# Performance work log

Hardware: AMD Instinct MI355X
Metric: run time of the kernel (lower is better)

Reference implementation:

```python
import jax, jax.numpy as jnp
import numpy as np
from jax import lax

OUT_SCALE = 0.001


def setup_inputs() -> dict:
    key = jax.random.key(0)
    kz, kx = jax.random.split(key)
    z = jax.random.normal(kz, (64, 256, 7, 7), dtype=jnp.float32)
    x = jax.random.normal(kx, (64, 256, 31, 31), dtype=jnp.float32)
    return {"z": z, "x": x}


def reference(z, x):
    # depthwise cross-correlation: each (batch, channel) slice of z is slid
    # over the matching slice of x. Implemented as a grouped conv with
    # feature_group_count = B*C, exactly mirroring torch F.conv2d(groups=B*C).
    B, C, kh, kw = z.shape
    H, W = x.shape[2], x.shape[3]
    x_r = x.reshape(1, B * C, H, W)           # [1, B*C, H, W]
    k_r = z.reshape(B * C, 1, kh, kw)          # [B*C, 1, kh, kw] (OIHW)
    out = lax.conv_general_dilated(
        x_r, k_r,
        window_strides=(1, 1),
        padding="VALID",
        feature_group_count=B * C,
        dimension_numbers=("NCHW", "OIHW", "NCHW"),
    )  # [1, B*C, H-kh+1, W-kw+1]
    out = out.reshape(B, C, out.shape[2], out.shape[3])
    return out * OUT_SCALE
```

## Files before the change

### kernel.cpp

```cpp
#include <hip/hip_runtime.h>


#define KH 7
#define KW 7
#define XW 31
#define OH 25
#define OW 25
#define NSLICE (64 * 256)
#define THREADS 256
#define NBLK 1536
#define RND 4
#define HALF_DW 3072
#define SLICE_X (XW * XW)
#define SLICE_O (OH * OW)
#define X_TOTAL_DW (NSLICE * SLICE_X)

__device__ __forceinline__ void gl_lds16(const float* g, float* l) {
    __builtin_amdgcn_global_load_lds(
        (const __attribute__((address_space(1))) void*)g,
        (__attribute__((address_space(3))) void*)l, 16, 0, 0);
}

__device__ __forceinline__ void stage3(const float* __restrict__ x,
                                       float* __restrict__ half,
                                       int sbase, int lane) {
    const int g0 = (sbase * SLICE_X) & ~3;
    #pragma unroll
    for (int k = 0; k < 12; ++k) {
        const int dw = k * 256 + lane * 4;
        gl_lds16(x + min(g0 + dw, X_TOTAL_DW - 4), half + dw);
    }
}

__global__ __launch_bounds__(THREADS, 6)
void xcorr_dw_kernel(const float* __restrict__ z,
                     const float* __restrict__ x,
                     float* __restrict__ out) {
    __shared__ float xs[2][HALF_DW];
    const int lane = threadIdx.x & 63;
    const int wv   = __builtin_amdgcn_readfirstlane(threadIdx.x >> 6);
    const int b    = blockIdx.x;

    if (wv == 3) {
        stage3(x, xs[0], 12 * b, lane);
        asm volatile("s_waitcnt vmcnt(0)" ::: "memory");
        __builtin_amdgcn_sched_barrier(0);
        #pragma unroll 1
        for (int r = 0; r < RND; ++r) {
            __builtin_amdgcn_s_barrier();
            if (r + 1 < RND) {
                stage3(x, xs[(r + 1) & 1], 12 * b + 3 * (r + 1), lane);
                asm volatile("s_waitcnt vmcnt(0)" ::: "memory");
                __builtin_amdgcn_sched_barrier(0);
            }
        }
    } else {
        const int h   = (lane >= OH) ? 1 : 0;
        const int oy  = h ? lane - OH : lane;
        const int c0  = h ? 13 : 0;
        const bool act = (lane < 2 * OH);
        #pragma unroll 1
        for (int r = 0; r < RND; ++r) {
            __builtin_amdgcn_s_barrier();
            const int sbase = 12 * b + 3 * r;
            const int s     = sbase + wv;
            if (s < NSLICE) {
                const int pre = (sbase * SLICE_X) & 3;
                float* __restrict__ buf = xs[r & 1] + pre + wv * SLICE_X;
                const float* __restrict__ zw = z + (size_t)s * (KH * KW);
                if (act) {
                    float acc[13] = {};
                    #pragma unroll
                    for (int i = 0; i < KH; ++i) {
                        const float* __restrict__ p = buf + (oy + i) * XW + c0;
                        float f[19];
                        #pragma unroll
                        for (int c = 0; c < 19; ++c) f[c] = p[c];
                        #pragma unroll
                        for (int j = 0; j < KW; ++j) {
                            const float w = zw[i * KW + j];
                            #pragma unroll
                            for (int c = 0; c < 13; ++c)
                                acc[c] = fmaf(f[c + j], w, acc[c]);
                        }
                    }
                    const int fb = oy * OW + c0;
                    #pragma unroll
                    for (int c = 0; c < 12; ++c) buf[fb + c] = acc[c] * 0.001f;
                    if (c0 == 0) buf[fb + 12] = acc[12] * 0.001f;
                }
                float* __restrict__ og = out + (size_t)s * SLICE_O;
                #pragma unroll
                for (int k = 0; k < 9; ++k) og[k * 64 + lane] = buf[k * 64 + lane];
                if (lane < SLICE_O - 576) og[576 + lane] = buf[576 + lane];
            }
        }
    }
}

extern "C" void kernel_launch(void* const* d_in, const int* in_sizes, int n_in,
                              void* d_out, int out_size, void* d_ws, size_t ws_size,
                              hipStream_t stream) {
    const float* z = (const float*)d_in[0];
    const float* x = (const float*)d_in[1];
    float* out = (float*)d_out;
    xcorr_dw_kernel<<<dim3(NBLK), dim3(THREADS), 0, stream>>>(z, x, out);
}
```

Baseline: 116.8 us.

## Replace loader-wave double-buffered pipeline with independent per-wave load-compute-store

The old design had one wave per block acting as a dedicated loader, feeding three compute waves through double-buffered LDS stages separated by block barriers over four rounds. Now each 128-thread block holds two waves, and each wave loads its own slice into a private LDS buffer, waits on vmcnt, computes and writes out. This removes block barriers and the mostly idle loader wave. Latency hiding now depends on many small resident blocks rather than explicit prefetch overlap. Block count rises to 8192, which adds launch and scheduling overhead.

```diff
diff --git a/kernel.cpp b/kernel.cpp
--- a/kernel.cpp
+++ b/kernel.cpp
@@ -7,10 +7,9 @@
 #define OH 25
 #define OW 25
 #define NSLICE (64 * 256)
-#define THREADS 256
-#define NBLK 1536
-#define RND 4
-#define HALF_DW 3072
+#define THREADS 128
+#define NBLK (NSLICE / 2)
+#define BUF_DW 1024
 #define SLICE_X (XW * XW)
 #define SLICE_O (OH * OW)
 #define X_TOTAL_DW (NSLICE * SLICE_X)
@@ -21,81 +20,63 @@
         (__attribute__((address_space(3))) void*)l, 16, 0, 0);
 }
 
-__device__ __forceinline__ void stage3(const float* __restrict__ x,
-                                       float* __restrict__ half,
-                                       int sbase, int lane) {
-    const int g0 = (sbase * SLICE_X) & ~3;
-    #pragma unroll
-    for (int k = 0; k < 12; ++k) {
-        const int dw = k * 256 + lane * 4;
-        gl_lds16(x + min(g0 + dw, X_TOTAL_DW - 4), half + dw);
-    }
-}
-
 __global__ __launch_bounds__(THREADS, 6)
 void xcorr_dw_kernel(const float* __restrict__ z,
                      const float* __restrict__ x,
                      float* __restrict__ out) {
-    __shared__ float xs[2][HALF_DW];
+    __shared__ float xs[2][BUF_DW];
     const int lane = threadIdx.x & 63;
     const int wv   = __builtin_amdgcn_readfirstlane(threadIdx.x >> 6);
-    const int b    = blockIdx.x;
+    float* __restrict__ buf = xs[wv];
 
-    if (wv == 3) {
-        stage3(x, xs[0], 12 * b, lane);
-        asm volatile("s_waitcnt vmcnt(0)" ::: "memory");
-        __builtin_amdgcn_sched_barrier(0);
-        #pragma unroll 1
-        for (int r = 0; r < RND; ++r) {
-            __builtin_amdgcn_s_barrier();
-            if (r + 1 < RND) {
-                stage3(x, xs[(r + 1) & 1], 12 * b + 3 * (r + 1), lane);
-                asm volatile("s_waitcnt vmcnt(0)" ::: "memory");
-                __builtin_amdgcn_sched_barrier(0);
+    const int s = blockIdx.x * 2 + wv;
+
+    const int g0r = s * SLICE_X;
+    const int pre = g0r & 3;
+    const int g0  = g0r - pre;
+    #pragma unroll
+    for (int k = 0; k < 4; ++k) {
+        const int dw = k * 256 + lane * 4;
+        gl_lds16(x + min(g0 + dw, X_TOTAL_DW - 4), buf + dw);
+    }
+
+    const float* __restrict__ zw = z + (size_t)s * (KH * KW);
+
+    const int h   = (lane >= OH) ? 1 : 0;
+    const int oy  = h ? lane - OH : lane;
+    const int c0  = h ? 13 : 0;
+    const bool act = (lane < 2 * OH);
+
+    asm volatile("s_waitcnt vmcnt(0)" ::: "memory");
+    __builtin_amdgcn_sched_barrier(0);
+
+    if (act) {
+        float acc[13] = {};
+        const float* __restrict__ xrow = buf + pre;
+        #pragma unroll
+        for (int i = 0; i < KH; ++i) {
+            const float* __restrict__ p = xrow + (oy + i) * XW + c0;
+            float f[19];
+            #pragma unroll
+            for (int c = 0; c < 19; ++c) f[c] = p[c];
+            #pragma unroll
+            for (int j = 0; j < KW; ++j) {
+                const float w = zw[i * KW + j];
+                #pragma unroll
+                for (int c = 0; c < 13; ++c)
+                    acc[c] = fmaf(f[c + j], w, acc[c]);
             }
         }
-    } else {
-        const int h   = (lane >= OH) ? 1 : 0;
-        const int oy  = h ? lane - OH : lane;
-        const int c0  = h ? 13 : 0;
-        const bool act = (lane < 2 * OH);
-        #pragma unroll 1
-        for (int r = 0; r < RND; ++r) {
-            __builtin_amdgcn_s_barrier();
-            const int sbase = 12 * b + 3 * r;
-            const int s     = sbase + wv;
-            if (s < NSLICE) {
-                const int pre = (sbase * SLICE_X) & 3;
-                float* __restrict__ buf = xs[r & 1] + pre + wv * SLICE_X;
-                const float* __restrict__ zw = z + (size_t)s * (KH * KW);
-                if (act) {
-                    float acc[13] = {};
-                    #pragma unroll
-                    for (int i = 0; i < KH; ++i) {
-                        const float* __restrict__ p = buf + (oy + i) * XW + c0;
-                        float f[19];
-                        #pragma unroll
-                        for (int c = 0; c < 19; ++c) f[c] = p[c];
-                        #pragma unroll
-                        for (int j = 0; j < KW; ++j) {
-                            const float w = zw[i * KW + j];
-                            #pragma unroll
-                            for (int c = 0; c < 13; ++c)
-                                acc[c] = fmaf(f[c + j], w, acc[c]);
-                        }
-                    }
-                    const int fb = oy * OW + c0;
-                    #pragma unroll
-                    for (int c = 0; c < 12; ++c) buf[fb + c] = acc[c] * 0.001f;
-                    if (c0 == 0) buf[fb + 12] = acc[12] * 0.001f;
-                }
-                float* __restrict__ og = out + (size_t)s * SLICE_O;
-                #pragma unroll
-                for (int k = 0; k < 9; ++k) og[k * 64 + lane] = buf[k * 64 + lane];
-                if (lane < SLICE_O - 576) og[576 + lane] = buf[576 + lane];
-            }
-        }
+        const int fb = oy * OW + c0;
+        #pragma unroll
+        for (int c = 0; c < 12; ++c) buf[fb + c] = acc[c] * 0.001f;
+        if (!h) buf[fb + 12] = acc[12] * 0.001f;
     }
+
+    float* __restrict__ og = out + (size_t)s * SLICE_O;
+    #pragma unroll
+    for (int k = 0; k < 9; ++k) og[k * 64 + lane] = buf[k * 64 + lane];
+    if (lane < SLICE_O - 576) og[576 + lane] = buf[576 + lane];
 }
 
 extern "C" void kernel_launch(void* const* d_in, const int* in_sizes, int n_in,
```

New measurement: 114.2 us. 1.02x faster.
